# Kernel optimization log

Measured on AMD Instinct MI355X. Metric: run time of the kernel, lower is better.

The kernel has to match this reference:

```python
import jax, jax.numpy as jnp
import numpy as np

B, S, E, H, D = 2, 1024, 512, 8, 64
M, V, L = 2048, 32000, 2
BLOCK, NRAND = 64, 3
NEG = -1e9


def _bigbird_block_mask(n, block, r, seed):
    """Block-level BigBird mask: 3-wide sliding window + global first/last block + r random blocks per row."""
    nb = n // block
    m = np.zeros((nb, nb), dtype=bool)
    idx = np.arange(nb)
    for off in (-1, 0, 1):
        j = idx + off
        ok = (j >= 0) & (j < nb)
        m[idx[ok], j[ok]] = True
    m[0, :] = True
    m[-1, :] = True
    m[:, 0] = True
    m[:, -1] = True
    rng = np.random.RandomState(seed)
    for i in range(nb):
        m[i, rng.choice(nb, size=min(r, nb), replace=False)] = True
    return np.kron(m, np.ones((block, block), dtype=bool))  # [n, n]

_CAUSAL = np.tril(np.ones((S, S), dtype=bool))
_SELF_MASKS = [jnp.asarray(_bigbird_block_mask(S, BLOCK, NRAND, 1000 + l) & _CAUSAL) for l in range(L)]
_CROSS_MASKS = [jnp.asarray(_bigbird_block_mask(S, BLOCK, NRAND, l)) for l in range(L)]  # connectivity_seed=lyr


def _layernorm(x, scale, bias, eps=1e-6):
    mu = jnp.mean(x, axis=-1, keepdims=True)
    var = jnp.mean(jnp.square(x - mu), axis=-1, keepdims=True)
    return (x - mu) * jax.lax.rsqrt(var + eps) * scale + bias


def _attend(x_q, x_kv, wq, wk, wv, wo, mask):
    # mask: [B,1,S,S] bool. bias=False multi-head attention, scaled by 1/sqrt(head_dim).
    q = jnp.einsum('bqe,ehd->bqhd', x_q, wq) * (1.0 / D ** 0.5)
    k = jnp.einsum('bke,ehd->bkhd', x_kv, wk)
    v = jnp.einsum('bke,ehd->bkhd', x_kv, wv)
    s = jnp.einsum('bqhd,bkhd->bhqk', q, k)
    s = jnp.where(mask, s, NEG)
    p = jax.nn.softmax(s, axis=-1)
    o = jnp.einsum('bhqk,bkhd->bqhd', p, v)
    return jnp.einsum('bqhd,hde->bqe', o, wo)


def setup_inputs() -> dict:
    key = jax.random.key(0)
    ks = jax.random.split(key, 20)
    def n(i, shape, s=0.02):
        return jax.random.normal(ks[i], shape, jnp.float32) * s
    inp = {}
    inp['encoded'] = jax.random.normal(ks[0], (B, S, E), jnp.float32)
    inp['src_padding_mask'] = jnp.ones((B, S, 1), jnp.float32)
    inp['targets'] = jax.random.randint(ks[1], (B, S), 0, V).astype(jnp.int32)
    inp['embed_table'] = jax.random.normal(ks[2], (V, E), jnp.float32)  # normal(stddev=1.0) init
    inp['pos_emb'] = n(3, (1, S, E))
    for name in ('ln1', 'ln2', 'ln3'):
        inp[name + '_s'] = jnp.ones((L, E), jnp.float32)
        inp[name + '_b'] = jnp.zeros((L, E), jnp.float32)
    inp['self_wq'] = n(4, (L, E, H, D)); inp['self_wk'] = n(5, (L, E, H, D))
    inp['self_wv'] = n(6, (L, E, H, D)); inp['self_wo'] = n(7, (L, H, D, E))
    inp['cross_wq'] = n(8, (L, E, H, D)); inp['cross_wk'] = n(9, (L, E, H, D))
    inp['cross_wv'] = n(10, (L, E, H, D)); inp['cross_wo'] = n(11, (L, H, D, E))
    inp['mlp_w1'] = n(12, (L, E, M)); inp['mlp_b1'] = jnp.zeros((L, M), jnp.float32)
    inp['mlp_w2'] = n(13, (L, M, E)); inp['mlp_b2'] = jnp.zeros((L, E), jnp.float32)
    inp['final_s'] = jnp.ones((E,), jnp.float32); inp['final_b'] = jnp.zeros((E,), jnp.float32)
    inp['logit_w'] = n(14, (E, V)); inp['logit_b'] = jnp.zeros((V,), jnp.float32)
    return inp


def reference(encoded, src_padding_mask, targets, embed_table, pos_emb,
              ln1_s, ln1_b, ln2_s, ln2_b, ln3_s, ln3_b,
              self_wq, self_wk, self_wv, self_wo,
              cross_wq, cross_wk, cross_wv, cross_wo,
              mlp_w1, mlp_b1, mlp_w2, mlp_b2,
              final_s, final_b, logit_w, logit_b):
    tgt_pad = targets > 0                       # [B,S] bool (computed pre-shift, as in source)
    src_pad = src_padding_mask[..., 0] > 0      # [B,S] bool
    shifted = jnp.pad(targets, ((0, 0), (1, 0)))[:, :-1]  # shift_right
    y = embed_table[shifted] + pos_emb[:, :S, :]          # [B,S,E]  (dropout deterministic)
    pq = tgt_pad[:, None, :, None]              # [B,1,S,1]
    self_pad = pq & tgt_pad[:, None, None, :]
    cross_pad = pq & src_pad[:, None, None, :]
    for lyr in range(L):
        self_mask = _SELF_MASKS[lyr][None, None] & self_pad   # [B,1,S,S]
        x = _layernorm(y, ln1_s[lyr], ln1_b[lyr])
        x = _attend(x, x, self_wq[lyr], self_wk[lyr], self_wv[lyr], self_wo[lyr], self_mask) + y
        cross_mask = _CROSS_MASKS[lyr][None, None] & cross_pad
        z = _layernorm(x, ln2_s[lyr], ln2_b[lyr])
        z = _attend(z, encoded, cross_wq[lyr], cross_wk[lyr], cross_wv[lyr], cross_wo[lyr], cross_mask) + x
        h = _layernorm(z, ln3_s[lyr], ln3_b[lyr])
        h = jax.nn.relu(h @ mlp_w1[lyr] + mlp_b1[lyr]) @ mlp_w2[lyr] + mlp_b2[lyr]
        y = z + h
    y = _layernorm(y, final_s, final_b)
    return y @ logit_w + logit_b                # [B,S,V]
```

## Files before the change

kernel.cpp:

```cpp
#include <hip/hip_runtime.h>
#include <hip/hip_bf16.h>
#include <stdint.h>

#define B_ 2
#define S_ 1024
#define E_ 512
#define H_ 8
#define D_ 64
#define M_ 2048
#define V_ 32000
#define L_ 2

typedef __hip_bfloat16 bf16;
typedef __attribute__((ext_vector_type(8))) short short8;
typedef __attribute__((ext_vector_type(4))) float f32x4;
typedef __attribute__((ext_vector_type(16))) float f32x16;
typedef __attribute__((ext_vector_type(4))) unsigned int uint4v;

__device__ inline unsigned int pack2bf(float lo, float hi) {
    __hip_bfloat16 a = __float2bfloat16(lo), b = __float2bfloat16(hi);
    unsigned short ua = *(unsigned short*)&a, ub = *(unsigned short*)&b;
    return (unsigned int)ua | ((unsigned int)ub << 16);
}

#define MT_N 624
#define MT_M 397
#define MT_UP   0x80000000u
#define MT_LOW  0x7fffffffu
#define MT_MAT  0x9908b0dfu

__device__ inline unsigned int mt_temper(unsigned int y) {
    y ^= y >> 11;
    y ^= (y << 7) & 0x9d2c5680u;
    y ^= (y << 15) & 0xefc60000u;
    y ^= y >> 18;
    return y;
}

__global__ __launch_bounds__(256)
void prep_kernel(const int* __restrict__ targets, const float* __restrict__ table,
                 const float* __restrict__ pos, float* __restrict__ y,
                 const float* __restrict__ enc, bf16* __restrict__ encb,
                 float* __restrict__ vmbase) {
    int bid = blockIdx.x, t = threadIdx.x;
    if (bid < 2048) {
        int s = bid & (S_ - 1), b = bid >> 10;
        int id = (s == 0) ? 0 : targets[b * S_ + s - 1];
        int c = t * 2;
        float2 e = *(const float2*)&table[(size_t)id * E_ + c];
        float2 p = *(const float2*)&pos[(size_t)s * E_ + c];
        float2 o = {e.x + p.x, e.y + p.y};
        *(float2*)&y[(size_t)bid * E_ + c] = o;
    } else if (bid < 3072) {
        int i = ((bid - 2048) * 256 + t) * 4;
        float4 v = *(const float4*)&enc[i];
        encb[i + 0] = __float2bfloat16(v.x);
        encb[i + 1] = __float2bfloat16(v.y);
        encb[i + 2] = __float2bfloat16(v.z);
        encb[i + 3] = __float2bfloat16(v.w);
    } else {
        vmbase[(bid - 3072) * 256 + t] = 0.0f;
    }
}

struct TP16 { const float* s[16]; bf16* d[16]; };
__global__ __launch_bounds__(256)
void tconv16m_kernel(TP16 p, unsigned char* masks) {
    __shared__ float Ts[32][33];
    __shared__ unsigned int mto[4][MT_N];
    __shared__ unsigned int mtn[4][MT_N];
    const int z = blockIdx.z;
    if (z == 16) {
        if (blockIdx.x != 0 || blockIdx.y != 0) return;
        const int w = threadIdx.x >> 6, lane = threadIdx.x & 63;
        const unsigned int seeds[4] = {1000u, 1001u, 0u, 1u};
        unsigned char* m = masks + w * 256;
        for (int idx = lane; idx < 256; idx += 64) {
            int i = idx >> 4, j = idx & 15;
            bool v = (j >= i - 1 && j <= i + 1) || i == 0 || i == 15 || j == 0 || j == 15;
            m[idx] = v ? 1 : 0;
        }
        if (lane == 0) {
            unsigned int s = seeds[w];
            for (int i = 0; i < MT_N; ++i) {
                mto[w][i] = s;
                s = 1812433253u * (s ^ (s >> 30)) + (unsigned int)(i + 1);
            }
        }
        __syncthreads();
        for (int i = lane; i < MT_N - MT_M; i += 64) {
            unsigned int y = (mto[w][i] & MT_UP) | (mto[w][i + 1] & MT_LOW);
            mtn[w][i] = mto[w][i + MT_M] ^ (y >> 1) ^ ((y & 1u) ? MT_MAT : 0u);
        }
        __syncthreads();
        for (int i = 227 + lane; i < 454; i += 64) {
            unsigned int y = (mto[w][i] & MT_UP) | (mto[w][i + 1] & MT_LOW);
            mtn[w][i] = mtn[w][i - 227] ^ (y >> 1) ^ ((y & 1u) ? MT_MAT : 0u);
        }
        __syncthreads();
        for (int i = 454 + lane; i < MT_N - 1; i += 64) {
            unsigned int y = (mto[w][i] & MT_UP) | (mto[w][i + 1] & MT_LOW);
            mtn[w][i] = mtn[w][i - 227] ^ (y >> 1) ^ ((y & 1u) ? MT_MAT : 0u);
        }
        __syncthreads();
        if (lane == 0) {
            unsigned int y = (mto[w][MT_N - 1] & MT_UP) | (mtn[w][0] & MT_LOW);
            mtn[w][MT_N - 1] = mtn[w][MT_M - 1] ^ (y >> 1) ^ ((y & 1u) ? MT_MAT : 0u);
        }
        __syncthreads();
        if (lane == 0) {
            int idx = 0;
            for (int i = 0; i < 16; ++i) {
                unsigned long long arr = 0xFEDCBA9876543210ULL;
                for (int k = 15; k > 0; --k) {
                    unsigned int mask = k;
                    mask |= mask >> 1; mask |= mask >> 2; mask |= mask >> 4;
                    unsigned int j;
                    for (;;) {
                        if (idx >= MT_N) {
                            int i2 = 0;
                            for (; i2 < MT_N - MT_M; ++i2) {
                                unsigned int y2 = (mtn[w][i2] & MT_UP) | (mtn[w][i2 + 1] & MT_LOW);
                                mtn[w][i2] = mtn[w][i2 + MT_M] ^ (y2 >> 1) ^ ((y2 & 1u) ? MT_MAT : 0u);
                            }
                            for (; i2 < MT_N - 1; ++i2) {
                                unsigned int y2 = (mtn[w][i2] & MT_UP) | (mtn[w][i2 + 1] & MT_LOW);
                                mtn[w][i2] = mtn[w][i2 - 227] ^ (y2 >> 1) ^ ((y2 & 1u) ? MT_MAT : 0u);
                            }
                            unsigned int y2 = (mtn[w][MT_N - 1] & MT_UP) | (mtn[w][0] & MT_LOW);
                            mtn[w][MT_N - 1] = mtn[w][MT_M - 1] ^ (y2 >> 1) ^ ((y2 & 1u) ? MT_MAT : 0u);
                            idx = 0;
                        }
                        j = mt_temper(mtn[w][idx++]) & mask;
                        if (j <= (unsigned int)k) break;
                    }
                    unsigned int a = (unsigned int)(arr >> (4 * k)) & 15u;
                    unsigned int bnib = (unsigned int)(arr >> (4 * j)) & 15u;
                    arr &= ~((15ULL << (4 * k)) | (15ULL << (4 * j)));
                    arr |= ((unsigned long long)a << (4 * j)) | ((unsigned long long)bnib << (4 * k));
                }
                m[i * 16 + ((arr >> 0) & 15)] = 1;
                m[i * 16 + ((arr >> 4) & 15)] = 1;
                m[i * 16 + ((arr >> 8) & 15)] = 1;
            }
        }
        return;
    }
    const float* W = p.s[z];
    bf16* Wt = p.d[z];
    int k0 = blockIdx.x * 32, n0 = blockIdx.y * 32;
    int lx = threadIdx.x & 31, ly = threadIdx.x >> 5;
    for (int r = ly; r < 32; r += 8)
        Ts[r][lx] = W[(size_t)(k0 + r) * E_ + n0 + lx];
    __syncthreads();
    for (int r = ly; r < 32; r += 8)
        Wt[(size_t)(n0 + r) * E_ + k0 + lx] = __float2bfloat16(Ts[lx][r]);
}

__global__ __launch_bounds__(256)
void tconv_mlp_kernel(const float* __restrict__ w1, const float* __restrict__ w2,
                      bf16* __restrict__ w1t, bf16* __restrict__ w2t) {
    __shared__ float Ts[32][33];
    int z = blockIdx.z;
    const float* W; bf16* Wt; int K, N, k0, n0;
    if (z < 2) {
        W = w1 + (size_t)z * E_ * M_; Wt = w1t + (size_t)z * E_ * M_;
        K = E_; N = M_; k0 = blockIdx.y * 32; n0 = blockIdx.x * 32;
    } else {
        W = w2 + (size_t)(z - 2) * M_ * E_; Wt = w2t + (size_t)(z - 2) * M_ * E_;
        K = M_; N = E_; k0 = blockIdx.x * 32; n0 = blockIdx.y * 32;
    }
    int lx = threadIdx.x & 31, ly = threadIdx.x >> 5;
    for (int r = ly; r < 32; r += 8)
        Ts[r][lx] = W[(size_t)(k0 + r) * N + n0 + lx];
    __syncthreads();
    for (int r = ly; r < 32; r += 8)
        Wt[(size_t)(n0 + r) * K + k0 + lx] = __float2bfloat16(Ts[lx][r]);
}

__global__ __launch_bounds__(256)
void tconv_kernel(const float* __restrict__ W, bf16* __restrict__ Wt, int K, int N) {
    __shared__ float Ts[32][33];
    int k0 = blockIdx.x * 32, n0 = blockIdx.y * 32;
    int lx = threadIdx.x & 31, ly = threadIdx.x >> 5;
    for (int r = ly; r < 32; r += 8)
        Ts[r][lx] = W[(size_t)(k0 + r) * N + n0 + lx];
    __syncthreads();
    for (int r = ly; r < 32; r += 8)
        Wt[(size_t)(n0 + r) * K + k0 + lx] = __float2bfloat16(Ts[lx][r]);
}

__global__ __launch_bounds__(256)
void ln_kernel(const float* __restrict__ x, bf16* __restrict__ y,
               const float* __restrict__ sc, const float* __restrict__ bi) {
    int row = blockIdx.x;
    int t = threadIdx.x;
    const float* xr = x + (size_t)row * E_;
    float2 v = *(const float2*)&xr[t * 2];
    float sum = v.x + v.y;
    float sq = v.x * v.x + v.y * v.y;
    for (int off = 32; off > 0; off >>= 1) {
        sum += __shfl_xor(sum, off);
        sq  += __shfl_xor(sq, off);
    }
    __shared__ float s0[4], s1[4];
    int w = t >> 6;
    if ((t & 63) == 0) { s0[w] = sum; s1[w] = sq; }
    __syncthreads();
    sum = s0[0] + s0[1] + s0[2] + s0[3];
    sq  = s1[0] + s1[1] + s1[2] + s1[3];
    float mu = sum * (1.0f / (float)E_);
    float var = sq * (1.0f / (float)E_) - mu * mu;
    float rs = rsqrtf(var + 1e-6f);
    float2 s2 = *(const float2*)&sc[t * 2];
    float2 b2 = *(const float2*)&bi[t * 2];
    bf16* yr = y + (size_t)row * E_ + t * 2;
    yr[0] = __float2bfloat16((v.x - mu) * rs * s2.x + b2.x);
    yr[1] = __float2bfloat16((v.y - mu) * rs * s2.y + b2.y);
}

template<int OBF, int FM, int VS, int FN = 4>
__global__ __launch_bounds__(256)
void gemm_mfma(const bf16* __restrict__ A, const bf16* __restrict__ Wt,
               const float* __restrict__ bias, const float* __restrict__ resid,
               void* __restrict__ Cv, int M, int N, int K, float alpha, int relu,
               float* __restrict__ vsum, int vlo)
{
    constexpr int BN = FN * 32;
    __shared__ bf16 As[FM * 32 * 64];
    __shared__ bf16 Bs[BN * 64];
    const int t = threadIdx.x;
    const int lane = t & 63, w = t >> 6;
    int m0, n0;
    {
        int nwg = gridDim.x * gridDim.y;
        int lin = blockIdx.x + gridDim.x * blockIdx.y;
        int q = nwg >> 3, r = nwg & 7;
        int xcd = lin & 7, off8 = lin >> 3;
        int swz = ((xcd < r) ? xcd * (q + 1) : r * (q + 1) + (xcd - r) * q) + off8;
        int gridM = gridDim.y;
        m0 = (swz % gridM) * (FM * 32);
        n0 = (swz / gridM) * BN;
    }
    const int wr = w >> 1, wc = w & 1;
    const int srow = w * 8 + (lane >> 3);
    const int sslot = lane & 7;
    f32x4 acc[FM][FN] = {};

    for (int k0 = 0; k0 < K; k0 += 64) {
        __syncthreads();
        #pragma unroll
        for (int i = 0; i < FM; ++i) {
            int r = i * 32 + srow;
            int gslot = sslot ^ (r & 7);
            const bf16* ga = A + (size_t)(m0 + r) * K + k0 + gslot * 8;
            __builtin_amdgcn_global_load_lds((const __attribute__((address_space(1))) void*)ga,
                                             (__attribute__((address_space(3))) void*)&As[r * 64 + sslot * 8],
                                             16, 0, 0);
        }
        #pragma unroll
        for (int i = 0; i < FN; ++i) {
            int r = i * 32 + srow;
            int gslot = sslot ^ (r & 7);
            const bf16* gb = Wt + (size_t)(n0 + r) * K + k0 + gslot * 8;
            __builtin_amdgcn_global_load_lds((const __attribute__((address_space(1))) void*)gb,
                                             (__attribute__((address_space(3))) void*)&Bs[r * 64 + sslot * 8],
                                             16, 0, 0);
        }
        __syncthreads();
        #pragma unroll
        for (int kk = 0; kk < 2; ++kk) {
            short8 af[FM], bq[FN];
            const int q = kk * 4 + (lane >> 4);
            #pragma unroll
            for (int m = 0; m < FM; ++m) {
                int r = wr * (FM * 16) + m * 16 + (lane & 15);
                af[m] = *(const short8*)&As[r * 64 + (q ^ (r & 7)) * 8];
            }
            #pragma unroll
            for (int n = 0; n < FN; ++n) {
                int r = wc * (FN * 16) + n * 16 + (lane & 15);
                bq[n] = *(const short8*)&Bs[r * 64 + (q ^ (r & 7)) * 8];
            }
            #pragma unroll
            for (int m = 0; m < FM; ++m)
                #pragma unroll
                for (int n = 0; n < FN; ++n)
                    acc[m][n] = __builtin_amdgcn_mfma_f32_16x16x32_bf16(bq[n], af[m], acc[m][n], 0, 0, 0);
        }
    }

    const int lr = lane >> 4, lc = lane & 15;
    float vpart[FN][4] = {};
    #pragma unroll
    for (int m = 0; m < FM; ++m) {
        int row = m0 + wr * (FM * 16) + m * 16 + lc;
        #pragma unroll
        for (int n = 0; n < FN; ++n) {
            int colb = n0 + wc * (FN * 16) + n * 16 + lr * 4;
            float v0 = acc[m][n][0] * alpha, v1 = acc[m][n][1] * alpha;
            float v2 = acc[m][n][2] * alpha, v3 = acc[m][n][3] * alpha;
            if (bias) {
                float4 bv = *(const float4*)&bias[colb];
                v0 += bv.x; v1 += bv.y; v2 += bv.z; v3 += bv.w;
            }
            if (relu) {
                v0 = fmaxf(v0, 0.0f); v1 = fmaxf(v1, 0.0f);
                v2 = fmaxf(v2, 0.0f); v3 = fmaxf(v3, 0.0f);
            }
            if (resid) {
                float4 rv = *(const float4*)&resid[(size_t)row * N + colb];
                v0 += rv.x; v1 += rv.y; v2 += rv.z; v3 += rv.w;
            }
            if (OBF) {
                uint2 pp = {pack2bf(v0, v1), pack2bf(v2, v3)};
                *(uint2*)((bf16*)Cv + (size_t)row * N + colb) = pp;
                if constexpr (VS) {
                    vpart[n][0] += __uint_as_float(pp.x << 16);
                    vpart[n][1] += __uint_as_float(pp.x & 0xffff0000u);
                    vpart[n][2] += __uint_as_float(pp.y << 16);
                    vpart[n][3] += __uint_as_float(pp.y & 0xffff0000u);
                }
            } else {
                float4 o = {v0, v1, v2, v3};
                *(float4*)((float*)Cv + (size_t)row * N + colb) = o;
            }
        }
    }
    if constexpr (VS) {
        int bidx = (m0 + wr * (FM * 16)) >> 10;
        #pragma unroll
        for (int n = 0; n < FN; ++n) {
            #pragma unroll
            for (int j = 0; j < 4; ++j) {
                float s = vpart[n][j];
                s += __shfl_xor(s, 1); s += __shfl_xor(s, 2);
                s += __shfl_xor(s, 4); s += __shfl_xor(s, 8);
                vpart[n][j] = s;
            }
            if (lc == 0) {
                int colb = n0 + wc * (FN * 16) + n * 16 + lr * 4;
                int rr = colb - vlo;
                if (rr >= 0) {
                    int g = rr >> 10, d = rr & 1023;
                    if (d < 512) {
                        float* dst = vsum + g * (B_ * 512) + bidx * 512 + d;
                        atomicAdd(dst + 0, vpart[n][0]);
                        atomicAdd(dst + 1, vpart[n][1]);
                        atomicAdd(dst + 2, vpart[n][2]);
                        atomicAdd(dst + 3, vpart[n][3]);
                    }
                }
            }
        }
    }
}

__global__ __launch_bounds__(128)
void attn_mfma(const bf16* __restrict__ qp, const bf16* __restrict__ kp,
               const bf16* __restrict__ vp, bf16* __restrict__ op,
               const unsigned char* __restrict__ bm,
               const int* __restrict__ targets, const float* __restrict__ srcmask,
               const float* __restrict__ vmean,
               int sq, int sk, int sv, int causal)
{
    __shared__ __align__(16) unsigned char lds[24592];
    unsigned long long* padb = (unsigned long long*)(lds + 24576);

    const int bid = blockIdx.x;
    const int qb = bid & 15, h = (bid >> 4) & 7, b = bid >> 7;
    const int tid = threadIdx.x;
    const int wq = tid >> 6, lane = tid & 63;
    const int h5 = lane >> 5, l31 = lane & 31;

    unsigned char* Ks = lds;
    unsigned char* Vt = lds + 8192;
    unsigned char* Qs = lds + 16384;

    #pragma unroll
    for (int j = 0; j < 4; ++j) {
        int r = wq * 32 + j * 8 + (lane >> 3);
        int g = (lane & 7) ^ (r & 7);
        const bf16* src = qp + (size_t)(b * S_ + qb * 64 + r) * sq + h * 64 + g * 8;
        __builtin_amdgcn_global_load_lds((const __attribute__((address_space(1))) void*)src,
            (__attribute__((address_space(3))) void*)(Qs + wq * 4096 + j * 1024 + lane * 16),
            16, 0, 0);
    }
    __syncthreads();
    short8 qfrag[4];
    {
        int qrow = wq * 32 + l31;
        #pragma unroll
        for (int t = 0; t < 4; ++t) {
            int c = (2 * t + h5) ^ (qrow & 7);
            qfrag[t] = *(const short8*)(Qs + qrow * 128 + c * 16);
        }
    }

    const int q_in = wq * 32 + l31;
    const int qg = qb * 64 + q_in;
    const bool padq = targets[b * S_ + qg] > 0;

    unsigned long long lstpk = 0ULL;
    int myn = 0;
    {
        int kbmax = causal ? qb : 15;
        for (int kb = 0; kb <= kbmax; ++kb)
            if (bm[qb * 16 + kb]) { lstpk |= ((unsigned long long)kb) << (4 * myn); ++myn; }
    }

    float mrun = -3.0e38f, lrun = 0.0f;
    f32x16 acc0 = {}, acc1 = {};

    for (int it = 0; it < myn; ++it) {
        int kb = (int)((lstpk >> (4 * it)) & 15ULL);
        #pragma unroll
        for (int j = 0; j < 4; ++j) {
            int r = j * 16 + wq * 8 + (lane >> 3);
            int g = (lane & 7) ^ (r & 7);
            const bf16* src = kp + (size_t)(b * S_ + kb * 64 + r) * sk + h * 64 + g * 8;
            __builtin_amdgcn_global_load_lds((const __attribute__((address_space(1))) void*)src,
                (__attribute__((address_space(3))) void*)(Ks + (j * 16 + wq * 8) * 128 + lane * 16),
                16, 0, 0);
        }
        #pragma unroll
        for (int itv = 0; itv < 2; ++itv) {
            int k2 = 2 * l31;
            int d0 = h5 * 8 + (wq * 2 + itv) * 16;
            const unsigned short* v0 = (const unsigned short*)vp +
                (size_t)(b * S_ + kb * 64 + k2) * sv + h * 64 + d0;
            short8 va = *(const short8*)v0;
            short8 vb = *(const short8*)(v0 + sv);
            #pragma unroll
            for (int j2 = 0; j2 < 8; ++j2) {
                int d = d0 + j2;
                unsigned int pkv = ((unsigned int)(unsigned short)va[j2]) |
                                   (((unsigned int)(unsigned short)vb[j2]) << 16);
                int off = d * 128 + (((k2 >> 3) ^ (d & 7)) * 16) + (k2 & 7) * 2;
                *(unsigned int*)(Vt + off) = pkv;
            }
        }
        if (wq == 0) {
            int pos = b * S_ + kb * 64 + lane;
            bool pk_ = srcmask ? (srcmask[pos] > 0.0f) : (targets[pos] > 0);
            unsigned long long bits = __ballot(pk_);
            if (lane == 0) padb[0] = bits;
        }
        __syncthreads();
        {
            bool diag = causal && (kb == qb);
            unsigned long long pb = padb[0];
            #pragma unroll
            for (int ks = 0; ks < 2; ++ks) {
                f32x16 sacc = {};
                #pragma unroll
                for (int t = 0; t < 4; ++t) {
                    int row = ks * 32 + l31;
                    int c = (2 * t + h5) ^ (row & 7);
                    short8 kfrag = *(const short8*)(Ks + row * 128 + c * 16);
                    sacc = __builtin_amdgcn_mfma_f32_32x32x16_bf16(kfrag, qfrag[t], sacc, 0, 0, 0);
                }
                float p[16];
                float mloc = -3.0e38f;
                #pragma unroll
                for (int r = 0; r < 16; ++r) {
                    int kl = ks * 32 + (r & 3) + 8 * (r >> 2) + 4 * h5;
                    bool ok = padq && (((pb >> kl) & 1ULL) != 0) && (!diag || kl <= q_in);
                    p[r] = ok ? sacc[r] * 0.125f : -1.0e9f;
                    mloc = fmaxf(mloc, p[r]);
                }
                mloc = fmaxf(mloc, __shfl_xor(mloc, 32));
                float mnew = fmaxf(mrun, mloc);
                float rescale = __expf(mrun - mnew);
                float lsum = 0.0f;
                #pragma unroll
                for (int r = 0; r < 16; ++r) { p[r] = __expf(p[r] - mnew); lsum += p[r]; }
                lsum += __shfl_xor(lsum, 32);
                lrun = lrun * rescale + lsum;
                mrun = mnew;
                acc0 *= rescale;
                acc1 *= rescale;
                unsigned int pk_hi[4][2], pk_lo[4][2];
                #pragma unroll
                for (int t4 = 0; t4 < 4; ++t4)
                    #pragma unroll
                    for (int u = 0; u < 2; ++u) {
                        float a = p[4 * t4 + 2 * u];
                        float c = p[4 * t4 + 2 * u + 1];
                        unsigned int ph = pack2bf(a, c);
                        float ah = __uint_as_float(ph << 16);
                        float ch = __uint_as_float(ph & 0xffff0000u);
                        pk_hi[t4][u] = ph;
                        pk_lo[t4][u] = pack2bf(a - ah, c - ch);
                    }
                #pragma unroll
                for (int Hh = 0; Hh < 2; ++Hh) {
                    unsigned int hu0 = (unsigned int)__shfl_xor((int)pk_hi[2 * Hh + 1][0], 32);
                    unsigned int hu1 = (unsigned int)__shfl_xor((int)pk_hi[2 * Hh + 1][1], 32);
                    unsigned int hl0 = (unsigned int)__shfl_xor((int)pk_hi[2 * Hh][0], 32);
                    unsigned int hl1 = (unsigned int)__shfl_xor((int)pk_hi[2 * Hh][1], 32);
                    uint4v hv = {h5 ? hu0 : pk_hi[2 * Hh][0],
                                 h5 ? hu1 : pk_hi[2 * Hh][1],
                                 h5 ? pk_hi[2 * Hh + 1][0] : hl0,
                                 h5 ? pk_hi[2 * Hh + 1][1] : hl1};
                    short8 bfrag_hi = __builtin_bit_cast(short8, hv);
                    unsigned int lu0 = (unsigned int)__shfl_xor((int)pk_lo[2 * Hh + 1][0], 32);
                    unsigned int lu1 = (unsigned int)__shfl_xor((int)pk_lo[2 * Hh + 1][1], 32);
                    unsigned int ll0 = (unsigned int)__shfl_xor((int)pk_lo[2 * Hh][0], 32);
                    unsigned int ll1 = (unsigned int)__shfl_xor((int)pk_lo[2 * Hh][1], 32);
                    uint4v lv = {h5 ? lu0 : pk_lo[2 * Hh][0],
                                 h5 ? lu1 : pk_lo[2 * Hh][1],
                                 h5 ? pk_lo[2 * Hh + 1][0] : ll0,
                                 h5 ? pk_lo[2 * Hh + 1][1] : ll1};
                    short8 bfrag_lo = __builtin_bit_cast(short8, lv);
                    #pragma unroll
                    for (int f = 0; f < 2; ++f) {
                        int row = f * 32 + l31;
                        int c = (4 * ks + 2 * Hh + h5) ^ (row & 7);
                        short8 vfrag = *(const short8*)(Vt + row * 128 + c * 16);
                        if (f == 0) {
                            acc0 = __builtin_amdgcn_mfma_f32_32x32x16_bf16(vfrag, bfrag_hi, acc0, 0, 0, 0);
                            acc0 = __builtin_amdgcn_mfma_f32_32x32x16_bf16(vfrag, bfrag_lo, acc0, 0, 0, 0);
                        } else {
                            acc1 = __builtin_amdgcn_mfma_f32_32x32x16_bf16(vfrag, bfrag_hi, acc1, 0, 0, 0);
                            acc1 = __builtin_amdgcn_mfma_f32_32x32x16_bf16(vfrag, bfrag_lo, acc1, 0, 0, 0);
                        }
                    }
                }
            }
        }
        __syncthreads();
    }

    bool okrow = mrun > -5.0e8f;
    float inv = okrow ? 1.0f / lrun : 0.0f;
    const float* vmp = vmean + (b * 8 + h) * 64;
    const float invS = 1.0f / (float)S_;
    unsigned short* orow = (unsigned short*)op + (size_t)(b * S_ + qg) * E_ + h * 64;
    #pragma unroll
    for (int f = 0; f < 2; ++f)
        #pragma unroll
        for (int t4 = 0; t4 < 4; ++t4)
            #pragma unroll
            for (int u = 0; u < 2; ++u) {
                int r = 4 * t4 + 2 * u;
                int d = f * 32 + 2 * u + 8 * t4 + 4 * h5;
                float a0 = f ? acc1[r] : acc0[r];
                float a1 = f ? acc1[r + 1] : acc0[r + 1];
                float v0 = a0 * inv;
                float v1 = a1 * inv;
                if (!okrow) { v0 = vmp[d] * invS; v1 = vmp[d + 1] * invS; }
                *(unsigned int*)(orow + d) = pack2bf(v0, v1);
            }
}

extern "C" void kernel_launch(void* const* d_in, const int* in_sizes, int n_in,
                              void* d_out, int out_size, void* d_ws, size_t ws_size,
                              hipStream_t stream)
{
    const float* encoded  = (const float*)d_in[0];
    const float* srcmask  = (const float*)d_in[1];
    const int*   targets  = (const int*)d_in[2];
    const float* table    = (const float*)d_in[3];
    const float* pos      = (const float*)d_in[4];
    const float* ln1_s = (const float*)d_in[5];
    const float* ln1_b = (const float*)d_in[6];
    const float* ln2_s = (const float*)d_in[7];
    const float* ln2_b = (const float*)d_in[8];
    const float* ln3_s = (const float*)d_in[9];
    const float* ln3_b = (const float*)d_in[10];
    const float* self_wq = (const float*)d_in[11];
    const float* self_wk = (const float*)d_in[12];
    const float* self_wv = (const float*)d_in[13];
    const float* self_wo = (const float*)d_in[14];
    const float* cross_wq = (const float*)d_in[15];
    const float* cross_wk = (const float*)d_in[16];
    const float* cross_wv = (const float*)d_in[17];
    const float* cross_wo = (const float*)d_in[18];
    const float* mlp_w1 = (const float*)d_in[19];
    const float* mlp_b1 = (const float*)d_in[20];
    const float* mlp_w2 = (const float*)d_in[21];
    const float* mlp_b2 = (const float*)d_in[22];
    const float* final_s = (const float*)d_in[23];
    const float* final_b = (const float*)d_in[24];
    const float* logit_w = (const float*)d_in[25];
    const float* logit_b = (const float*)d_in[26];
    float* out = (float*)d_out;

    char* ws = (char*)d_ws;
    unsigned char* masks = (unsigned char*)ws;
    size_t off = 1024;
    auto alloc = [&](size_t bytes) {
        char* p = ws + off;
        off += (bytes + 255) & ~(size_t)255;
        return p;
    };
    const size_t RS = (size_t)B_ * S_;
    const size_t EE = (size_t)E_ * E_;
    float* y    = (float*)alloc(RS * E_ * 4);
    float* xb   = (float*)alloc(RS * E_ * 4);
    float* zb   = (float*)alloc(RS * E_ * 4);
    bf16* lnb   = (bf16*)alloc(RS * E_ * 2);
    bf16* qkvb  = (bf16*)alloc(RS * 3 * E_ * 2);
    bf16* kvb   = (bf16*)alloc(RS * 4 * E_ * 2);
    bf16* qb2   = (bf16*)alloc(RS * E_ * 2);
    bf16* ob    = (bf16*)alloc(RS * E_ * 2);
    bf16* hid   = (bf16*)alloc(RS * M_ * 2);
    bf16* encb  = (bf16*)alloc(RS * E_ * 2);
    float* vmbase = (float*)alloc(4096 * 4);
    float* vms = vmbase;
    float* vmc = vmbase + 2048;
    bf16* qkv_t = (bf16*)alloc((size_t)L_ * 3 * EE * 2);
    bf16* swo_t = (bf16*)alloc((size_t)L_ * EE * 2);
    bf16* cq_t  = (bf16*)alloc((size_t)L_ * EE * 2);
    bf16* ckv_t = (bf16*)alloc((size_t)L_ * 2 * EE * 2);
    bf16* cwo_t = (bf16*)alloc((size_t)L_ * EE * 2);
    bf16* w1_t  = (bf16*)alloc((size_t)L_ * E_ * M_ * 2);
    bf16* w2_t  = (bf16*)alloc((size_t)L_ * M_ * E_ * 2);
    bf16* wl_t  = (bf16*)alloc((size_t)E_ * V_ * 2);

    const int R = (int)RS;

    prep_kernel<<<3088, 256, 0, stream>>>(targets, table, pos, y, encoded, encb, vmbase);

    {
        TP16 p;
        for (int l = 0; l < L_; ++l) {
            p.s[l * 8 + 0] = self_wq + l * EE;  p.d[l * 8 + 0] = qkv_t + (size_t)l * 3 * EE + 0 * EE;
            p.s[l * 8 + 1] = self_wk + l * EE;  p.d[l * 8 + 1] = qkv_t + (size_t)l * 3 * EE + 1 * EE;
            p.s[l * 8 + 2] = self_wv + l * EE;  p.d[l * 8 + 2] = qkv_t + (size_t)l * 3 * EE + 2 * EE;
            p.s[l * 8 + 3] = self_wo + l * EE;  p.d[l * 8 + 3] = swo_t + (size_t)l * EE;
            p.s[l * 8 + 4] = cross_wq + l * EE; p.d[l * 8 + 4] = cq_t + (size_t)l * EE;
            p.s[l * 8 + 5] = cross_wk + l * EE; p.d[l * 8 + 5] = ckv_t + (size_t)l * 2 * EE + 0 * EE;
            p.s[l * 8 + 6] = cross_wv + l * EE; p.d[l * 8 + 6] = ckv_t + (size_t)l * 2 * EE + 1 * EE;
            p.s[l * 8 + 7] = cross_wo + l * EE; p.d[l * 8 + 7] = cwo_t + (size_t)l * EE;
        }
        dim3 gf(E_ / 32, E_ / 32, 17);
        tconv16m_kernel<<<gf, 256, 0, stream>>>(p, masks);
        dim3 gm(64, 16, 4);
        tconv_mlp_kernel<<<gm, 256, 0, stream>>>(mlp_w1, mlp_w2, w1_t, w2_t);
        dim3 g3(E_ / 32, V_ / 32, 1);
        tconv_kernel<<<g3, 256, 0, stream>>>(logit_w, wl_t, E_, V_);
    }

    dim3 gqkv2(3 * E_ / 128, R / 64);
    dim3 gkv42(4 * E_ / 128, R / 64);
    dim3 gp2(E_ / 128, R / 64);
    dim3 g12(M_ / 128, R / 64);
    dim3 gl8(V_ / 256, R / 64);
    const int attn_grid = B_ * H_ * 16;

    gemm_mfma<1, 2, 1><<<gkv42, 256, 0, stream>>>(encb, ckv_t, nullptr, nullptr, kvb, R, 4 * E_, E_, 1.0f, 0, vmc, 512);

    for (int l = 0; l < L_; ++l) {
        ln_kernel<<<R, 256, 0, stream>>>(y, lnb, ln1_s + l * E_, ln1_b + l * E_);
        gemm_mfma<1, 2, 1><<<gqkv2, 256, 0, stream>>>(lnb, qkv_t + (size_t)l * 3 * EE, nullptr, nullptr, qkvb, R, 3 * E_, E_, 1.0f, 0, vms + l * (B_ * 512), 1024);
        attn_mfma<<<attn_grid, 128, 0, stream>>>(qkvb, qkvb + E_, qkvb + 2 * E_, ob, masks + l * 256,
                                                 targets, nullptr, vms + l * (B_ * 512), 3 * E_, 3 * E_, 3 * E_, 1);
        gemm_mfma<0, 2, 0><<<gp2, 256, 0, stream>>>(ob, swo_t + (size_t)l * EE, nullptr, y, xb, R, E_, E_, 1.0f, 0, nullptr, 0);
        ln_kernel<<<R, 256, 0, stream>>>(xb, lnb, ln2_s + l * E_, ln2_b + l * E_);
        gemm_mfma<1, 2, 0><<<gp2, 256, 0, stream>>>(lnb, cq_t + (size_t)l * EE, nullptr, nullptr, qb2, R, E_, E_, 1.0f, 0, nullptr, 0);
        attn_mfma<<<attn_grid, 128, 0, stream>>>(qb2, kvb + (size_t)l * 2 * E_, kvb + (size_t)l * 2 * E_ + E_, ob,
                                                 masks + (2 + l) * 256, targets, srcmask,
                                                 vmc + l * (B_ * 512), E_, 4 * E_, 4 * E_, 0);
        gemm_mfma<0, 2, 0><<<gp2, 256, 0, stream>>>(ob, cwo_t + (size_t)l * EE, nullptr, xb, zb, R, E_, E_, 1.0f, 0, nullptr, 0);
        ln_kernel<<<R, 256, 0, stream>>>(zb, lnb, ln3_s + l * E_, ln3_b + l * E_);
        gemm_mfma<1, 2, 0><<<g12, 256, 0, stream>>>(lnb, w1_t + (size_t)l * E_ * M_, mlp_b1 + (size_t)l * M_, nullptr, hid, R, M_, E_, 1.0f, 1, nullptr, 0);
        gemm_mfma<0, 2, 0><<<gp2, 256, 0, stream>>>(hid, w2_t + (size_t)l * M_ * E_, mlp_b2 + (size_t)l * E_, zb, y, R, E_, M_, 1.0f, 0, nullptr, 0);
    }

    ln_kernel<<<R, 256, 0, stream>>>(y, lnb, final_s, final_b);
    gemm_mfma<0, 2, 0, 8><<<gl8, 256, 0, stream>>>(lnb, wl_t, logit_b, nullptr, out, R, V_, E_, 1.0f, 0, nullptr, 0);
}
```

Baseline: 726.4 us.

## Double-buffer LDS tiles in MFMA GEMM to overlap global loads with compute

The GEMM kernel now allocates two LDS buffers for the A and W tiles. It issues the async global-to-LDS loads for the next K-step before running the MFMAs on the current one, with a single waitcnt plus barrier per iteration instead of two syncthreads. The aim is to hide global memory latency behind matrix math. The cost is double the LDS use per workgroup, which can lower occupancy.

Result: slower. 749.6 us (+3.2%).

```diff
diff --git a/kernel.cpp b/kernel.cpp
--- a/kernel.cpp
+++ b/kernel.cpp
@@ -227,8 +227,10 @@
                float* __restrict__ vsum, int vlo)
 {
     constexpr int BN = FN * 32;
-    __shared__ bf16 As[FM * 32 * 64];
-    __shared__ bf16 Bs[BN * 64];
+    constexpr int ASZ = FM * 32 * 64;
+    constexpr int BSZ = BN * 64;
+    __shared__ bf16 As[2 * ASZ];
+    __shared__ bf16 Bs[2 * BSZ];
     const int t = threadIdx.x;
     const int lane = t & 63, w = t >> 6;
     int m0, n0;
@@ -247,15 +249,14 @@
     const int sslot = lane & 7;
     f32x4 acc[FM][FN] = {};
 
-    for (int k0 = 0; k0 < K; k0 += 64) {
-        __syncthreads();
+    auto stage = [&](int buf, int k0) {
         #pragma unroll
         for (int i = 0; i < FM; ++i) {
             int r = i * 32 + srow;
             int gslot = sslot ^ (r & 7);
             const bf16* ga = A + (size_t)(m0 + r) * K + k0 + gslot * 8;
             __builtin_amdgcn_global_load_lds((const __attribute__((address_space(1))) void*)ga,
-                                             (__attribute__((address_space(3))) void*)&As[r * 64 + sslot * 8],
+                                             (__attribute__((address_space(3))) void*)&As[buf * ASZ + r * 64 + sslot * 8],
                                              16, 0, 0);
         }
         #pragma unroll
@@ -264,10 +265,22 @@
             int gslot = sslot ^ (r & 7);
             const bf16* gb = Wt + (size_t)(n0 + r) * K + k0 + gslot * 8;
             __builtin_amdgcn_global_load_lds((const __attribute__((address_space(1))) void*)gb,
-                                             (__attribute__((address_space(3))) void*)&Bs[r * 64 + sslot * 8],
+                                             (__attribute__((address_space(3))) void*)&Bs[buf * BSZ + r * 64 + sslot * 8],
                                              16, 0, 0);
         }
-        __syncthreads();
+    };
+
+    stage(0, 0);
+    asm volatile("s_waitcnt vmcnt(0)" ::: "memory");
+    __builtin_amdgcn_s_barrier();
+    __builtin_amdgcn_sched_barrier(0);
+
+    int cur = 0;
+    for (int k0 = 0; k0 < K; k0 += 64) {
+        if (k0 + 64 < K) stage(cur ^ 1, k0 + 64);
+        __builtin_amdgcn_sched_barrier(0);
+        const bf16* Asb = &As[cur * ASZ];
+        const bf16* Bsb = &Bs[cur * BSZ];
         #pragma unroll
         for (int kk = 0; kk < 2; ++kk) {
             short8 af[FM], bq[FN];
@@ -275,12 +288,12 @@
             #pragma unroll
             for (int m = 0; m < FM; ++m) {
                 int r = wr * (FM * 16) + m * 16 + (lane & 15);
-                af[m] = *(const short8*)&As[r * 64 + (q ^ (r & 7)) * 8];
+                af[m] = *(const short8*)&Asb[r * 64 + (q ^ (r & 7)) * 8];
             }
             #pragma unroll
             for (int n = 0; n < FN; ++n) {
                 int r = wc * (FN * 16) + n * 16 + (lane & 15);
-                bq[n] = *(const short8*)&Bs[r * 64 + (q ^ (r & 7)) * 8];
+                bq[n] = *(const short8*)&Bsb[r * 64 + (q ^ (r & 7)) * 8];
             }
             #pragma unroll
             for (int m = 0; m < FM; ++m)
@@ -288,6 +301,10 @@
                 for (int n = 0; n < FN; ++n)
                     acc[m][n] = __builtin_amdgcn_mfma_f32_16x16x32_bf16(bq[n], af[m], acc[m][n], 0, 0, 0);
         }
+        asm volatile("s_waitcnt vmcnt(0)" ::: "memory");
+        __builtin_amdgcn_s_barrier();
+        __builtin_amdgcn_sched_barrier(0);
+        cur ^= 1;
     }
 
     const int lr = lane >> 4, lc = lane & 15;
```
